# Optimization experiments

Hardware: AMD Instinct MI355X
Metric: run time of the kernel (lower is better)

The kernel has to match this reference:

```python
import jax, jax.numpy as jnp
import numpy as np

EXPANSION_K = 5
N_CENTERS = 8192
DIM = 512
BATCH = 4096


def setup_inputs() -> dict:
    key = jax.random.key(0)
    k1, k2, k3 = jax.random.split(key, 3)
    z = jax.random.normal(k1, (BATCH, DIM), dtype=jnp.float32)
    # learned PMField parameters: center positions and gravitational masses
    centers = jax.random.normal(k2, (N_CENTERS, DIM), dtype=jnp.float32)
    mus = jax.random.uniform(k3, (N_CENTERS,), dtype=jnp.float32, minval=0.1, maxval=1.0)
    return {"z": z, "centers": centers, "mus": mus}


def reference(z, centers, mus):
    # --- compute_center_attractions ---
    # torch.cdist(z, centers) -> Euclidean distances (B, N), computed GEMM-style
    sq = (
        jnp.sum(z * z, axis=-1, keepdims=True)          # (B, 1)
        + jnp.sum(centers * centers, axis=-1)[None, :]   # (1, N)
        - 2.0 * (z @ centers.T)                          # (B, N)
    )
    dists = jnp.sqrt(jnp.maximum(sq, 0.0))
    attractions = mus[None, :] / (dists ** 2 + 1e-6)     # (B, N)

    # --- expand_query ---
    top_vals, top_idx = jax.lax.top_k(attractions, EXPANSION_K)  # (B, k)
    weights = jax.nn.softmax(top_vals, axis=1)                    # (B, k)
    expanded_centers = centers[top_idx]                           # gather -> (B, k, D)
    comb = jnp.einsum("bkd,bk->bd", expanded_centers, weights)   # weighted center combine
    expanded_z = 0.7 * z + 0.3 * comb                             # (B, D)
    return expanded_z, attractions
```

## Files before the change

kernel.cpp:

```cpp
#include <hip/hip_runtime.h>
#include <math.h>

#define BATCH 4096
#define NC    8192
#define DIM   512
#define KEXP  5
#define NCAND 10

using bf16x8 = __attribute__((ext_vector_type(8))) short;
using f32x4  = __attribute__((ext_vector_type(4))) float;

__device__ unsigned short g_zbf[BATCH * DIM];
__device__ unsigned short g_cbf[NC * DIM];
__device__ float g_z2[BATCH];
__device__ float g_c2[NC];

__device__ __forceinline__ unsigned short rtne_bf16(float f) {
  unsigned u = __float_as_uint(f);
  u += 0x7FFFu + ((u >> 16) & 1u);
  return (unsigned short)(u >> 16);
}

__device__ __forceinline__ void gload16(const void* g, void* l) {
  __builtin_amdgcn_global_load_lds(
      (const __attribute__((address_space(1))) void*)g,
      (__attribute__((address_space(3))) void*)l, 16, 0, 0);
}

__global__ __launch_bounds__(256) void convert_kernel(const float* __restrict__ z,
                                                      const float* __restrict__ c) {
  const size_t i = ((size_t)blockIdx.x * 256 + threadIdx.x) * 8;
  const size_t zn = (size_t)BATCH * DIM;
  const float* src;
  unsigned short* dst;
  size_t off;
  if (i < zn) { src = z; dst = g_zbf; off = i; }
  else        { src = c; dst = g_cbf; off = i - zn; }
  float4 a = *(const float4*)(src + off);
  float4 b = *(const float4*)(src + off + 4);
  uint4 o;
  o.x = (unsigned)rtne_bf16(a.x) | ((unsigned)rtne_bf16(a.y) << 16);
  o.y = (unsigned)rtne_bf16(a.z) | ((unsigned)rtne_bf16(a.w) << 16);
  o.z = (unsigned)rtne_bf16(b.x) | ((unsigned)rtne_bf16(b.y) << 16);
  o.w = (unsigned)rtne_bf16(b.z) | ((unsigned)rtne_bf16(b.w) << 16);
  *(uint4*)(dst + off) = o;
}

__global__ __launch_bounds__(128) void norms_kernel(const float* __restrict__ z,
                                                    const float* __restrict__ c) {
  int row = blockIdx.x;
  const float* src;
  float* dst;
  if (row < BATCH) { src = z + (size_t)row * DIM; dst = g_z2 + row; }
  else             { src = c + (size_t)(row - BATCH) * DIM; dst = g_c2 + (row - BATCH); }
  int t = threadIdx.x;
  float4 v = ((const float4*)src)[t];
  double acc = (double)v.x * v.x + (double)v.y * v.y + (double)v.z * v.z + (double)v.w * v.w;
#pragma unroll
  for (int off = 32; off > 0; off >>= 1) acc += __shfl_down(acc, off);
  __shared__ double wsum[2];
  if ((t & 63) == 0) wsum[t >> 6] = acc;
  __syncthreads();
  if (t == 0) *dst = (float)(wsum[0] + wsum[1]);
}

#define BM  128
#define BN  128
#define BKK 64

__global__ __launch_bounds__(256) void attr_bf16(const float* __restrict__ mus,
                                                 float* __restrict__ att) {
  __shared__ __align__(16) unsigned short Ah[BM * BKK];
  __shared__ __align__(16) unsigned short Bh[BM * BKK];

  const int tid  = threadIdx.x;
  const int lane = tid & 63;
  const int wid  = tid >> 6;
  const int wm   = wid >> 1;
  const int wn   = wid & 1;

  const int flat = blockIdx.y * gridDim.x + blockIdx.x;
  const int swz  = (flat & 7) * 256 + (flat >> 3);
  const int col0 = (swz & 63) * BN;
  const int row0 = (swz >> 6) * BM;

  f32x4 acc[4][4] = {};

  const unsigned short* Ag = g_zbf + (size_t)row0 * DIM;
  const unsigned short* Bg = g_cbf + (size_t)col0 * DIM;

  const int crow = lane >> 3;
  const int gsw  = (lane & 7) ^ crow;

  for (int k0 = 0; k0 < DIM; k0 += BKK) {
#pragma unroll
    for (int j = 0; j < 4; ++j) {
      const int base_row = (wid * 4 + j) * 8;
      const int r = base_row + crow;
      gload16(Ag + (size_t)r * DIM + k0 + gsw * 8, Ah + base_row * 64);
      gload16(Bg + (size_t)r * DIM + k0 + gsw * 8, Bh + base_row * 64);
    }
    __syncthreads();

#pragma unroll
    for (int kk = 0; kk < 2; ++kk) {
      bf16x8 fa[4], fb[4];
#pragma unroll
      for (int i = 0; i < 4; ++i) {
        const int r = wm * 64 + i * 16 + (lane & 15);
        const int g = (kk * 4 + (lane >> 4)) ^ (r & 7);
        fa[i] = *(const bf16x8*)((const char*)Ah + r * 128 + g * 16);
      }
#pragma unroll
      for (int j2 = 0; j2 < 4; ++j2) {
        const int r = wn * 64 + j2 * 16 + (lane & 15);
        const int g = (kk * 4 + (lane >> 4)) ^ (r & 7);
        fb[j2] = *(const bf16x8*)((const char*)Bh + r * 128 + g * 16);
      }
#pragma unroll
      for (int i = 0; i < 4; ++i)
#pragma unroll
        for (int j2 = 0; j2 < 4; ++j2)
          acc[i][j2] = __builtin_amdgcn_mfma_f32_16x16x32_bf16(fa[i], fb[j2], acc[i][j2], 0, 0, 0);
    }
    __syncthreads();
  }

#pragma unroll
  for (int i = 0; i < 4; ++i) {
    const int mrow = row0 + wm * 64 + i * 16 + (lane >> 4) * 4;
    float zz[4];
#pragma unroll
    for (int r = 0; r < 4; ++r) zz[r] = g_z2[mrow + r];
#pragma unroll
    for (int j = 0; j < 4; ++j) {
      const int gc = col0 + wn * 64 + j * 16 + (lane & 15);
      const float cc = g_c2[gc];
      const float mu = mus[gc];
#pragma unroll
      for (int r = 0; r < 4; ++r) {
        float t   = __fadd_rn(zz[r], cc);
        float sq  = __fsub_rn(t, __fmul_rn(2.0f, acc[i][j][r]));
        float d   = sqrtf(fmaxf(sq, 0.0f));
        float den = __fadd_rn(__fmul_rn(d, d), 1e-6f);
        att[(size_t)(mrow + r) * NC + gc] = __fdiv_rn(mu, den);
      }
    }
  }
}

__global__ __launch_bounds__(256) void topk_kernel(const float* __restrict__ att,
                                                   const float* __restrict__ z,
                                                   const float* __restrict__ centers,
                                                   const float* __restrict__ mus,
                                                   float* __restrict__ out) {
  const int lane = threadIdx.x & 63;
  const int row  = blockIdx.x * 4 + (threadIdx.x >> 6);
  const float4* arow4 = (const float4*)(att + (size_t)row * NC);

  float cmv[8]; int cmi[8];
#pragma unroll
  for (int c = 0; c < 8; ++c) {
    float bv = -INFINITY; int bi = 0x7FFFFFFF;
#pragma unroll
    for (int q = 0; q < 4; ++q) {
      float4 v = arow4[c * 256 + q * 64 + lane];
      const int ib = c * 1024 + q * 256 + lane * 4;
      if (v.x > bv) { bv = v.x; bi = ib + 0; }
      if (v.y > bv) { bv = v.y; bi = ib + 1; }
      if (v.z > bv) { bv = v.z; bi = ib + 2; }
      if (v.w > bv) { bv = v.w; bi = ib + 3; }
    }
    cmv[c] = bv; cmi[c] = bi;
  }

  int selIdx[NCAND];
#pragma unroll
  for (int s = 0; s < NCAND; ++s) selIdx[s] = -1;

#pragma unroll
  for (int it = 0; it < NCAND; ++it) {
    float v = cmv[0]; int i = cmi[0];
#pragma unroll
    for (int c = 1; c < 8; ++c)
      if (cmv[c] > v || (cmv[c] == v && cmi[c] < i)) { v = cmv[c]; i = cmi[c]; }
#pragma unroll
    for (int off = 32; off > 0; off >>= 1) {
      float ov = __shfl_xor(v, off);
      int   oi = __shfl_xor(i, off);
      if (ov > v || (ov == v && oi < i)) { v = ov; i = oi; }
    }
    selIdx[it] = i;

    const int ol = (i >> 2) & 63;
    const int oc = i >> 10;
    if (lane == ol) {
      float nv = -INFINITY; int ni = 0x7FFFFFFF;
#pragma unroll
      for (int q = 0; q < 4; ++q) {
        float4 v4 = arow4[oc * 256 + q * 64 + lane];
        float vv[4] = {v4.x, v4.y, v4.z, v4.w};
#pragma unroll
        for (int e = 0; e < 4; ++e) {
          const int idx = oc * 1024 + q * 256 + lane * 4 + e;
          bool skip = false;
#pragma unroll
          for (int s = 0; s < NCAND; ++s) skip |= (idx == selIdx[s]);
          if (!skip && vv[e] > nv) { nv = vv[e]; ni = idx; }
        }
      }
#pragma unroll
      for (int c = 0; c < 8; ++c) if (c == oc) { cmv[c] = nv; cmi[c] = ni; }
    }
  }

  const float* zrow = z + (size_t)row * DIM;
  const int d0 = lane * 8;
  const float4 za = *(const float4*)(zrow + d0);
  const float4 zb = *(const float4*)(zrow + d0 + 4);
  const float myz2 = g_z2[row];

  float exv[NCAND];
#pragma unroll
  for (int c = 0; c < NCAND; ++c) {
    const int ci = selIdx[c];
    const float* cp = centers + (size_t)ci * DIM + d0;
    float4 ca = *(const float4*)(cp);
    float4 cb = *(const float4*)(cp + 4);
    double p = (double)za.x * ca.x + (double)za.y * ca.y +
               (double)za.z * ca.z + (double)za.w * ca.w +
               (double)zb.x * cb.x + (double)zb.y * cb.y +
               (double)zb.z * cb.z + (double)zb.w * cb.w;
#pragma unroll
    for (int off = 32; off > 0; off >>= 1) p += __shfl_xor(p, off);
    float dotf = (float)p;
    float t   = __fadd_rn(myz2, g_c2[ci]);
    float sq  = __fsub_rn(t, __fmul_rn(2.0f, dotf));
    float d   = sqrtf(fmaxf(sq, 0.0f));
    float den = __fadd_rn(__fmul_rn(d, d), 1e-6f);
    exv[c] = __fdiv_rn(mus[ci], den);
  }

  bool used[NCAND];
#pragma unroll
  for (int c = 0; c < NCAND; ++c) used[c] = false;
  float tv[KEXP]; int tix[KEXP];
#pragma unroll
  for (int s = 0; s < KEXP; ++s) {
    float bv = -INFINITY; int bi = 0x7FFFFFFF; int bc = 0;
#pragma unroll
    for (int c = 0; c < NCAND; ++c) {
      if (!used[c] && (exv[c] > bv || (exv[c] == bv && selIdx[c] < bi))) {
        bv = exv[c]; bi = selIdx[c]; bc = c;
      }
    }
#pragma unroll
    for (int c = 0; c < NCAND; ++c) if (c == bc) used[c] = true;
    tv[s] = bv; tix[s] = bi;
  }

  float m = tv[0];
  float w[KEXP];
  float s = 0.0f;
#pragma unroll
  for (int k = 0; k < KEXP; ++k) { w[k] = expf(tv[k] - m); s += w[k]; }
#pragma unroll
  for (int k = 0; k < KEXP; ++k) w[k] /= s;

  float comb[8] = {0, 0, 0, 0, 0, 0, 0, 0};
#pragma unroll
  for (int k = 0; k < KEXP; ++k) {
    const float* cp = centers + (size_t)tix[k] * DIM + d0;
    float4 a = *(const float4*)(cp);
    float4 b = *(const float4*)(cp + 4);
    comb[0] += w[k] * a.x; comb[1] += w[k] * a.y;
    comb[2] += w[k] * a.z; comb[3] += w[k] * a.w;
    comb[4] += w[k] * b.x; comb[5] += w[k] * b.y;
    comb[6] += w[k] * b.z; comb[7] += w[k] * b.w;
  }
  const float zv[8] = {za.x, za.y, za.z, za.w, zb.x, zb.y, zb.z, zb.w};
  float o[8];
#pragma unroll
  for (int e = 0; e < 8; ++e)
    o[e] = __fadd_rn(__fmul_rn(0.7f, zv[e]), __fmul_rn(0.3f, comb[e]));
  *(float4*)(out + (size_t)row * DIM + d0)     = *(float4*)&o[0];
  *(float4*)(out + (size_t)row * DIM + d0 + 4) = *(float4*)&o[4];
}

extern "C" void kernel_launch(void* const* d_in, const int* in_sizes, int n_in,
                              void* d_out, int out_size, void* d_ws, size_t ws_size,
                              hipStream_t stream) {
  const float* z       = (const float*)d_in[0];
  const float* centers = (const float*)d_in[1];
  const float* mus     = (const float*)d_in[2];
  float* out      = (float*)d_out;
  float* expanded = out;
  float* att      = out + (size_t)BATCH * DIM;

  convert_kernel<<<(BATCH + NC) * DIM / (256 * 8), 256, 0, stream>>>(z, centers);
  norms_kernel<<<BATCH + NC, 128, 0, stream>>>(z, centers);
  dim3 grid(NC / BN, BATCH / BM);
  attr_bf16<<<grid, 256, 0, stream>>>(mus, att);
  topk_kernel<<<BATCH / 4, 256, 0, stream>>>(att, z, centers, mus, expanded);
}
```

Measured before the change: 172.4 us.

## Replace rescan-based candidate selection with per-lane packed top-4 lists

```diff
diff --git a/kernel.cpp b/kernel.cpp
--- a/kernel.cpp
+++ b/kernel.cpp
@@ -9,6 +9,7 @@
 
 using bf16x8 = __attribute__((ext_vector_type(8))) short;
 using f32x4  = __attribute__((ext_vector_type(4))) float;
+typedef unsigned long long u64;
 
 __device__ unsigned short g_zbf[BATCH * DIM];
 __device__ unsigned short g_cbf[NC * DIM];
@@ -149,68 +150,57 @@
   }
 }
 
-__global__ __launch_bounds__(256) void topk_kernel(const float* __restrict__ att,
-                                                   const float* __restrict__ z,
-                                                   const float* __restrict__ centers,
-                                                   const float* __restrict__ mus,
-                                                   float* __restrict__ out) {
+__global__ __launch_bounds__(256, 4) void topk_kernel(const float* __restrict__ att,
+                                                      const float* __restrict__ z,
+                                                      const float* __restrict__ centers,
+                                                      const float* __restrict__ mus,
+                                                      float* __restrict__ out) {
+  __shared__ int selLds[4][16];
   const int lane = threadIdx.x & 63;
-  const int row  = blockIdx.x * 4 + (threadIdx.x >> 6);
+  const int wv   = threadIdx.x >> 6;
+  const int row  = blockIdx.x * 4 + wv;
   const float4* arow4 = (const float4*)(att + (size_t)row * NC);
 
-  float cmv[8]; int cmi[8];
+  u64 k[8][4];
 #pragma unroll
   for (int c = 0; c < 8; ++c) {
-    float bv = -INFINITY; int bi = 0x7FFFFFFF;
+#pragma unroll
+    for (int j = 0; j < 4; ++j) k[c][j] = 0ull;
 #pragma unroll
     for (int q = 0; q < 4; ++q) {
-      float4 v = arow4[c * 256 + q * 64 + lane];
-      const int ib = c * 1024 + q * 256 + lane * 4;
-      if (v.x > bv) { bv = v.x; bi = ib + 0; }
-      if (v.y > bv) { bv = v.y; bi = ib + 1; }
-      if (v.z > bv) { bv = v.z; bi = ib + 2; }
-      if (v.w > bv) { bv = v.w; bi = ib + 3; }
-    }
-    cmv[c] = bv; cmi[c] = bi;
-  }
-
-  int selIdx[NCAND];
-#pragma unroll
-  for (int s = 0; s < NCAND; ++s) selIdx[s] = -1;
-
-#pragma unroll
+      float4 v4 = arow4[c * 256 + q * 64 + lane];
+      const unsigned ib = (unsigned)(c * 1024 + q * 256 + lane * 4);
+      const float vv[4] = {v4.x, v4.y, v4.z, v4.w};
+#pragma unroll
+      for (int e = 0; e < 4; ++e) {
+        u64 nk = ((u64)__float_as_uint(vv[e]) << 32) | (u64)(0xFFFFFFFFu - (ib + e));
+        bool g0 = nk > k[c][0], g1 = nk > k[c][1], g2 = nk > k[c][2], g3 = nk > k[c][3];
+        u64 t0 = k[c][0], t1 = k[c][1], t2 = k[c][2];
+        k[c][0] = g0 ? nk : k[c][0];
+        k[c][1] = g0 ? t0 : (g1 ? nk : k[c][1]);
+        k[c][2] = g1 ? t1 : (g2 ? nk : k[c][2]);
+        k[c][3] = g2 ? t2 : (g3 ? nk : k[c][3]);
+      }
+    }
+  }
+
   for (int it = 0; it < NCAND; ++it) {
-    float v = cmv[0]; int i = cmi[0];
-#pragma unroll
-    for (int c = 1; c < 8; ++c)
-      if (cmv[c] > v || (cmv[c] == v && cmi[c] < i)) { v = cmv[c]; i = cmi[c]; }
+    u64 b = k[0][0];
+#pragma unroll
+    for (int c = 1; c < 8; ++c) b = (k[c][0] > b) ? k[c][0] : b;
 #pragma unroll
     for (int off = 32; off > 0; off >>= 1) {
-      float ov = __shfl_xor(v, off);
-      int   oi = __shfl_xor(i, off);
-      if (ov > v || (ov == v && oi < i)) { v = ov; i = oi; }
-    }
-    selIdx[it] = i;
-
-    const int ol = (i >> 2) & 63;
-    const int oc = i >> 10;
-    if (lane == ol) {
-      float nv = -INFINITY; int ni = 0x7FFFFFFF;
-#pragma unroll
-      for (int q = 0; q < 4; ++q) {
-        float4 v4 = arow4[oc * 256 + q * 64 + lane];
-        float vv[4] = {v4.x, v4.y, v4.z, v4.w};
-#pragma unroll
-        for (int e = 0; e < 4; ++e) {
-          const int idx = oc * 1024 + q * 256 + lane * 4 + e;
-          bool skip = false;
-#pragma unroll
-          for (int s = 0; s < NCAND; ++s) skip |= (idx == selIdx[s]);
-          if (!skip && vv[e] > nv) { nv = vv[e]; ni = idx; }
-        }
-      }
-#pragma unroll
-      for (int c = 0; c < 8; ++c) if (c == oc) { cmv[c] = nv; cmi[c] = ni; }
+      u64 o = __shfl_xor(b, off);
+      b = (o > b) ? o : b;
+    }
+    if (lane == 0) selLds[wv][it] = (int)(0xFFFFFFFFu - (unsigned)(b & 0xFFFFFFFFu));
+#pragma unroll
+    for (int c = 0; c < 8; ++c) {
+      bool hit = (k[c][0] == b);
+      k[c][0] = hit ? k[c][1] : k[c][0];
+      k[c][1] = hit ? k[c][2] : k[c][1];
+      k[c][2] = hit ? k[c][3] : k[c][2];
+      k[c][3] = hit ? 0ull    : k[c][3];
     }
   }
 
@@ -220,20 +210,30 @@
   const float4 zb = *(const float4*)(zrow + d0 + 4);
   const float myz2 = g_z2[row];
 
-  float exv[NCAND];
+  double p[NCAND];
+  int cidx[NCAND];
 #pragma unroll
   for (int c = 0; c < NCAND; ++c) {
-    const int ci = selIdx[c];
-    const float* cp = centers + (size_t)ci * DIM + d0;
+    cidx[c] = selLds[wv][c];
+    const float* cp = centers + (size_t)cidx[c] * DIM + d0;
     float4 ca = *(const float4*)(cp);
     float4 cb = *(const float4*)(cp + 4);
-    double p = (double)za.x * ca.x + (double)za.y * ca.y +
-               (double)za.z * ca.z + (double)za.w * ca.w +
-               (double)zb.x * cb.x + (double)zb.y * cb.y +
-               (double)zb.z * cb.z + (double)zb.w * cb.w;
-#pragma unroll
-    for (int off = 32; off > 0; off >>= 1) p += __shfl_xor(p, off);
-    float dotf = (float)p;
+    p[c] = (double)za.x * ca.x + (double)za.y * ca.y +
+           (double)za.z * ca.z + (double)za.w * ca.w +
+           (double)zb.x * cb.x + (double)zb.y * cb.y +
+           (double)zb.z * cb.z + (double)zb.w * cb.w;
+  }
+#pragma unroll
+  for (int off = 32; off > 0; off >>= 1) {
+#pragma unroll
+    for (int c = 0; c < NCAND; ++c) p[c] += __shfl_xor(p[c], off);
+  }
+
+  float exv[NCAND];
+#pragma unroll
+  for (int c = 0; c < NCAND; ++c) {
+    const int ci = cidx[c];
+    float dotf = (float)p[c];
     float t   = __fadd_rn(myz2, g_c2[ci]);
     float sq  = __fsub_rn(t, __fmul_rn(2.0f, dotf));
     float d   = sqrtf(fmaxf(sq, 0.0f));
@@ -241,21 +241,19 @@
     exv[c] = __fdiv_rn(mus[ci], den);
   }
 
-  bool used[NCAND];
-#pragma unroll
-  for (int c = 0; c < NCAND; ++c) used[c] = false;
+  unsigned used = 0;
   float tv[KEXP]; int tix[KEXP];
 #pragma unroll
   for (int s = 0; s < KEXP; ++s) {
     float bv = -INFINITY; int bi = 0x7FFFFFFF; int bc = 0;
 #pragma unroll
     for (int c = 0; c < NCAND; ++c) {
-      if (!used[c] && (exv[c] > bv || (exv[c] == bv && selIdx[c] < bi))) {
-        bv = exv[c]; bi = selIdx[c]; bc = c;
-      }
-    }
-#pragma unroll
-    for (int c = 0; c < NCAND; ++c) if (c == bc) used[c] = true;
+      bool ok = (used & (1u << c)) == 0;
+      if (ok && (exv[c] > bv || (exv[c] == bv && cidx[c] < bi))) {
+        bv = exv[c]; bi = cidx[c]; bc = c;
+      }
+    }
+    used |= (1u << bc);
     tv[s] = bv; tix[s] = bi;
   }
 
@@ -263,20 +261,20 @@
   float w[KEXP];
   float s = 0.0f;
 #pragma unroll
-  for (int k = 0; k < KEXP; ++k) { w[k] = expf(tv[k] - m); s += w[k]; }
-#pragma unroll
-  for (int k = 0; k < KEXP; ++k) w[k] /= s;
+  for (int kk = 0; kk < KEXP; ++kk) { w[kk] = expf(tv[kk] - m); s += w[kk]; }
+#pragma unroll
+  for (int kk = 0; kk < KEXP; ++kk) w[kk] /= s;
 
   float comb[8] = {0, 0, 0, 0, 0, 0, 0, 0};
 #pragma unroll
-  for (int k = 0; k < KEXP; ++k) {
-    const float* cp = centers + (size_t)tix[k] * DIM + d0;
+  for (int kk = 0; kk < KEXP; ++kk) {
+    const float* cp = centers + (size_t)tix[kk] * DIM + d0;
     float4 a = *(const float4*)(cp);
-    float4 b = *(const float4*)(cp + 4);
-    comb[0] += w[k] * a.x; comb[1] += w[k] * a.y;
-    comb[2] += w[k] * a.z; comb[3] += w[k] * a.w;
-    comb[4] += w[k] * b.x; comb[5] += w[k] * b.y;
-    comb[6] += w[k] * b.z; comb[7] += w[k] * b.w;
+    float4 bq = *(const float4*)(cp + 4);
+    comb[0] += w[kk] * a.x;  comb[1] += w[kk] * a.y;
+    comb[2] += w[kk] * a.z;  comb[3] += w[kk] * a.w;
+    comb[4] += w[kk] * bq.x; comb[5] += w[kk] * bq.y;
+    comb[6] += w[kk] * bq.z; comb[7] += w[kk] * bq.w;
   }
   const float zv[8] = {za.x, za.y, za.z, za.w, zb.x, zb.y, zb.z, zb.w};
   float o[8];
```

Result: faster. 155.1 us (-10.0%).
